# Performance work log

Hardware: AMD Instinct MI355X
Metric: run time of the kernel (lower is better)

The kernel has to match this reference:

```python
import jax, jax.numpy as jnp
import numpy as np

NEG_SLOPE = 0.2

def _gc(inp, adj, W, b):
    # Kipf GraphConvolution: adj @ (inp @ W) + b
    return adj @ (inp @ W) + b

def _lrelu(x):
    return jnp.where(x >= 0, x, NEG_SLOPE * x)

def setup_inputs() -> dict:
    key = jax.random.key(0)
    ks = jax.random.split(key, 24)
    Nx, Ny, Fx, Fy, D1, C = 8192, 4096, 512, 256, 256, 64
    s = 0.05
    inp = {
        "hx1": jax.random.uniform(ks[0], (Nx, Nx), jnp.float32) / Nx,
        "hx2": jax.random.uniform(ks[1], (Nx, Ny), jnp.float32) / Ny,
        "x0": jax.random.normal(ks[2], (Nx, Fx), jnp.float32),
        "hy1": jax.random.uniform(ks[3], (Ny, Ny), jnp.float32) / Ny,
        "hy2": jax.random.uniform(ks[4], (Ny, Nx), jnp.float32) / Nx,
        "y0": jax.random.normal(ks[5], (Ny, Fy), jnp.float32),
        "alpha": jnp.float32(0.6),
        "beta": jnp.float32(0.4),
        # weights/biases of the 8 GraphConvolution layers
        "Wx1a": jax.random.normal(ks[6], (Fx, D1), jnp.float32) * s,
        "bx1a": jnp.zeros((D1,), jnp.float32),
        "Wx1b": jax.random.normal(ks[7], (Fy, D1), jnp.float32) * s,
        "bx1b": jnp.zeros((D1,), jnp.float32),
        "Wx2a": jax.random.normal(ks[8], (D1, C), jnp.float32) * s,
        "bx2a": jnp.zeros((C,), jnp.float32),
        "Wx2b": jax.random.normal(ks[9], (D1, C), jnp.float32) * s,
        "bx2b": jnp.zeros((C,), jnp.float32),
        "Wy1a": jax.random.normal(ks[10], (Fy, D1), jnp.float32) * s,
        "by1a": jnp.zeros((D1,), jnp.float32),
        "Wy1b": jax.random.normal(ks[11], (Fx, D1), jnp.float32) * s,
        "by1b": jnp.zeros((D1,), jnp.float32),
        "Wy2a": jax.random.normal(ks[12], (D1, C), jnp.float32) * s,
        "by2a": jnp.zeros((C,), jnp.float32),
        "Wy2b": jax.random.normal(ks[13], (D1, C), jnp.float32) * s,
        "by2b": jnp.zeros((C,), jnp.float32),
    }
    return inp

def reference(hx1, hx2, x0, hy1, hy2, y0, alpha, beta,
              Wx1a, bx1a, Wx1b, bx1b, Wx2a, bx2a, Wx2b, bx2b,
              Wy1a, by1a, Wy1b, by1b, Wy2a, by2a, Wy2b, by2b):
    # layer 1
    x1 = _lrelu(_gc(x0, hx1, Wx1a, bx1a) * alpha + _gc(y0, hx2, Wx1b, bx1b) * (1 - alpha))
    y1 = _lrelu(_gc(y0, hy1, Wy1a, by1a) * beta + _gc(x0, hy2, Wy1b, by1b) * (1 - beta))
    # layer 2
    x2 = _lrelu(_gc(x1, hx1, Wx2a, bx2a) * alpha + _gc(y1, hx2, Wx2b, bx2b) * (1 - alpha))
    y_pre = _gc(y1, hy1, Wy2a, by2a) * beta + _gc(x1, hy2, Wy2b, by2b) * (1 - beta)
    y2 = _lrelu(y_pre)
    h_hat = jax.nn.sigmoid(x2 @ y2.T)            # [Nx, Ny]
    x_output = jax.nn.log_softmax(x2, axis=1)    # [Nx, nclass]
    return (h_hat, x_output)
```

## Files before the change

kernel.cpp:

```cpp
#include <hip/hip_runtime.h>

typedef unsigned short u16;
typedef unsigned char u8;
typedef long i64;
typedef __attribute__((ext_vector_type(8))) short bf16x8;
typedef __attribute__((ext_vector_type(4))) float f32x4;
typedef __attribute__((ext_vector_type(8))) u16 u16x8;
typedef __attribute__((ext_vector_type(4))) u16 u16x4;
typedef __attribute__((ext_vector_type(4))) float f4;

#define DEVI static __device__ __forceinline__

DEVI u16 f2b(float f) { __bf16 h = (__bf16)f; return __builtin_bit_cast(u16, h); }
DEVI float b2f(u16 h) { unsigned u = ((unsigned)h) << 16; return __builtin_bit_cast(float, u); }

DEVI int pk8(float a, float b, float c, float d) {
  int w = __builtin_amdgcn_cvt_pk_fp8_f32(a, b, 0, false);
  return __builtin_amdgcn_cvt_pk_fp8_f32(c, d, w, true);
}

DEVI void gload16(const void* g, void* l) {
  __builtin_amdgcn_global_load_lds((const __attribute__((address_space(1))) void*)g,
                                   (__attribute__((address_space(3))) void*)l, 16, 0, 0);
}

__global__ __launch_bounds__(1024)
void gemmF_k(const float* __restrict__ xA0, const float* __restrict__ xA1,
             const u8* __restrict__ xB0, const u8* __restrict__ xB1,
             u8* __restrict__ xA0f8, u8* __restrict__ xA1f8,
             int xK0, int xK1, int xL0, int xL1, u16* __restrict__ xC, size_t xMN,
             const float* __restrict__ yA0, const float* __restrict__ yA1,
             const u8* __restrict__ yB0, const u8* __restrict__ yB1,
             u8* __restrict__ yA0f8, u8* __restrict__ yA1f8,
             int yK0, int yK1, int yL0, int yL1, u16* __restrict__ yC, size_t yMN)
{
  constexpr int BM = 128, BK = 64;
  constexpr int LDA = 72;
  constexpr int ASZ = BM * LDA;
  constexpr int BSZ = 256 * BK;
  constexpr int BUFSZ = ASZ + BSZ;
  constexpr float SADJ = 8192.f;
  __shared__ __align__(16) u8 lds[4 * BUFSZ];

  const int tid = threadIdx.x, lane = tid & 63, wave = tid >> 6;
  const int wm = (wave >> 2) * 32, wn = (wave & 3) * 64;
  const int lgrp = lane >> 4, lrow = lane & 15;

  const int flat = blockIdx.x;

  const float *A0, *A1; const u8 *B0, *B1; u8 *A0f8, *A1f8;
  int K0, K1, L0, L1; u16* Cout; size_t MN; int m0, z;
  if (flat < 256) {
    const int s = ((flat & 7) << 5) | (flat >> 3);
    A0=xA0; A1=xA1; B0=xB0; B1=xB1; A0f8=xA0f8; A1f8=xA1f8;
    K0=xK0; K1=xK1; L0=xL0; L1=xL1; Cout=xC; MN=xMN;
    m0 = (s & 63) * BM; z = s >> 6;
  } else {
    const int f2 = flat - 256;
    const int s = ((f2 & 7) << 5) | (f2 >> 3);
    A0=yA0; A1=yA1; B0=yB0; B1=yB1; A0f8=yA0f8; A1f8=yA1f8;
    K0=yK0; K1=yK1; L0=yL0; L1=yL1; Cout=yC; MN=yMN;
    m0 = (s & 31) * BM; z = s >> 5;
  }

  const int nt0 = L0 >> 6, NT = nt0 + (L1 >> 6);

  const int r0 = tid >> 4;
  const int cf = (tid & 15) << 2;

  f32x4 acc[2][4];
#pragma unroll
  for (int m = 0; m < 2; ++m)
#pragma unroll
    for (int n = 0; n < 4; ++n) acc[m][n] = (f32x4){0.f, 0.f, 0.f, 0.f};

  f4 rA0[2], rA1[2];
  int pw0[2], pw1[2];

  auto tileinfo = [&](int t, const float*& Ap, const u8*& Bp, u8*& Af8, int& Kj, int& kk) {
    if (t < nt0) { Ap = A0; Bp = B0; Af8 = A0f8; Kj = K0; kk = z * L0 + (t << 6); }
    else         { Ap = A1; Bp = B1; Af8 = A1f8; Kj = K1; kk = z * L1 + ((t - nt0) << 6); }
  };

  auto loadA = [&](int t, f4 (&r)[2]) {
    const float* Ap; const u8* Bp; u8* Af8; int Kj, kk;
    tileinfo(t, Ap, Bp, Af8, Kj, kk);
#pragma unroll
    for (int j = 0; j < 2; ++j) {
      const int rr = j * 64 + r0;
      r[j] = __builtin_nontemporal_load(
          (const f4*)(Ap + (size_t)(m0 + rr) * Kj + kk + cf));
    }
  };

  auto loadB = [&](int t) {
    const float* Ap; const u8* Bp; u8* Af8; int Kj, kk;
    tileinfo(t, Ap, Bp, Af8, Kj, kk);
    u8* sB = &lds[(t & 3) * BUFSZ] + ASZ;
    const int off = tid * 16;
    const int r = off >> 6, c = off & 63;
    gload16(Bp + (size_t)r * Kj + kk + (c ^ (((r >> 1) & 3) << 4)), sB + off);
  };

  auto writeLDS = [&](int t, f4 (&r)[2], int (&pw)[2]) {
    u8* sA = &lds[(t & 3) * BUFSZ];
#pragma unroll
    for (int j = 0; j < 2; ++j) {
      const int rr = j * 64 + r0;
      pw[j] = pk8(r[j][0] * SADJ, r[j][1] * SADJ, r[j][2] * SADJ, r[j][3] * SADJ);
      *(int*)&sA[rr * LDA + cf] = pw[j];
    }
  };

  auto storeCopy = [&](int t, int (&pw)[2]) {
    const float* Ap; const u8* Bp; u8* Af8; int Kj, kk;
    tileinfo(t, Ap, Bp, Af8, Kj, kk);
#pragma unroll
    for (int j = 0; j < 2; ++j) {
      const int rr = j * 64 + r0;
      *(int*)(Af8 + (size_t)(m0 + rr) * Kj + kk + cf) = pw[j];
    }
  };

  auto compute = [&](int t) {
    const u8* sA = &lds[(t & 3) * BUFSZ];
    const u8* sB = sA + ASZ;
    __builtin_amdgcn_s_setprio(1);
#pragma unroll
    for (int ks = 0; ks < 2; ++ks) {
      i64 a[2], b[4];
#pragma unroll
      for (int m = 0; m < 2; ++m) {
        const int r = wm + m * 16 + lrow;
        a[m] = *(const i64*)&sA[r * LDA + ks * 32 + lgrp * 8];
      }
#pragma unroll
      for (int n = 0; n < 4; ++n) {
        const int r = wn + n * 16 + lrow;
        b[n] = *(const i64*)&sB[r * BK + ((ks * 32 + lgrp * 8) ^ (((r >> 1) & 3) << 4))];
      }
#pragma unroll
      for (int m = 0; m < 2; ++m)
#pragma unroll
        for (int n = 0; n < 4; ++n)
          acc[m][n] = __builtin_amdgcn_mfma_f32_16x16x32_fp8_fp8(a[m], b[n], acc[m][n], 0, 0, 0);
    }
    __builtin_amdgcn_s_setprio(0);
  };

  loadA(0, rA0); loadB(0);
  loadA(1, rA1); loadB(1);

  for (int t = 0; t < NT; t += 2) {
    if (t == 0) asm volatile("s_waitcnt vmcnt(0)" ::: "memory");
    else        asm volatile("s_waitcnt vmcnt(4)" ::: "memory");
    writeLDS(t, rA0, pw0);
    writeLDS(t + 1, rA1, pw1);
    asm volatile("s_waitcnt lgkmcnt(0)" ::: "memory");
    asm volatile("s_barrier" ::: "memory");
    if (t + 2 < NT) { loadA(t + 2, rA0); loadB(t + 2); }
    if (t + 3 < NT) { loadA(t + 3, rA1); loadB(t + 3); }
    storeCopy(t, pw0);
    storeCopy(t + 1, pw1);
    compute(t);
    compute(t + 1);
  }

  u16* Cp = Cout + (size_t)z * MN;
#pragma unroll
  for (int n = 0; n < 4; ++n) {
    const int c = wn + n * 16 + lrow;
#pragma unroll
    for (int m = 0; m < 2; ++m) {
      const int rb = m0 + wm + m * 16 + lgrp * 4;
#pragma unroll
      for (int q = 0; q < 4; ++q)
        Cp[(size_t)(rb + q) * 256 + c] = f2b(acc[m][n][q]);
    }
  }
}

__global__ __launch_bounds__(256)
void gemm8_k(const u8* __restrict__ xA0, const u8* __restrict__ xA1,
             const u8* __restrict__ xB0, const u8* __restrict__ xB1,
             int xK0, int xK1, int xL0, int xL1, u16* __restrict__ xC, size_t xMN,
             const u8* __restrict__ yA0, const u8* __restrict__ yA1,
             const u8* __restrict__ yB0, const u8* __restrict__ yB1,
             int yK0, int yK1, int yL0, int yL1, u16* __restrict__ yC, size_t yMN)
{
  constexpr int BM = 128, BK = 128, BN = 64;
  constexpr int MR = 4, NR = 2;
  constexpr int ASZ = BM * BK, BSZ = BN * BK;
  __shared__ __align__(16) u8 lds[3 * (ASZ + BSZ)];

  const int tid = threadIdx.x, lane = tid & 63, wave = tid >> 6;
  const int wm = (wave >> 1) * 64, wn = (wave & 1) * 32;
  const int lgrp = lane >> 4, lrow = lane & 15;

  const int flat = blockIdx.x;

  const u8 *A0, *A1, *B0, *B1; int K0, K1, L0, L1; u16* Cw; size_t MN;
  int m0, z;
  if (flat < 512) {
    const int s = ((flat & 7) << 6) | (flat >> 3);
    A0=xA0; A1=xA1; B0=xB0; B1=xB1; K0=xK0; K1=xK1; L0=xL0; L1=xL1; Cw=xC; MN=xMN;
    m0 = (s & 63) * BM; z = s >> 6;
  } else {
    const int f2 = flat - 512;
    const int s = ((f2 & 7) << 6) | (f2 >> 3);
    A0=yA0; A1=yA1; B0=yB0; B1=yB1; K0=yK0; K1=yK1; L0=yL0; L1=yL1; Cw=yC; MN=yMN;
    m0 = (s & 31) * BM; z = s >> 5;
  }

  const int nt0 = L0 >> 7, NT = nt0 + (L1 >> 7);

  f32x4 acc[MR][NR];
#pragma unroll
  for (int m = 0; m < MR; ++m)
#pragma unroll
    for (int n = 0; n < NR; ++n) acc[m][n] = (f32x4){0.f, 0.f, 0.f, 0.f};

  auto stage = [&](int buf, int t) {
    const u8* Ap; const u8* Bp; int Kj, kk;
    if (t < nt0) { Ap = A0; Bp = B0; Kj = K0; kk = z * L0 + (t << 7); }
    else         { Ap = A1; Bp = B1; Kj = K1; kk = z * L1 + ((t - nt0) << 7); }
    u8* sA = &lds[buf * (ASZ + BSZ)];
    u8* sB = sA + ASZ;
#pragma unroll
    for (int i = 0; i < ASZ / 4096; ++i) {
      const int off = i * 4096 + tid * 16;
      const int r = off >> 7, c = off & 127;
      gload16(Ap + (size_t)(m0 + r) * Kj + kk + (c ^ ((r & 7) << 4)), sA + off);
    }
#pragma unroll
    for (int i = 0; i < BSZ / 4096; ++i) {
      const int off = i * 4096 + tid * 16;
      const int r = off >> 7, c = off & 127;
      gload16(Bp + (size_t)r * Kj + kk + (c ^ ((r & 7) << 4)), sB + off);
    }
  };

  auto compute = [&](int buf) {
    const u8* sA = &lds[buf * (ASZ + BSZ)];
    const u8* sB = sA + ASZ;
    __builtin_amdgcn_s_setprio(1);
#pragma unroll
    for (int ks = 0; ks < 4; ++ks) {
      i64 a[MR], b[NR];
#pragma unroll
      for (int m = 0; m < MR; ++m) {
        const int r = wm + m * 16 + lrow;
        a[m] = *(const i64*)&sA[r * BK + ((ks * 32 + lgrp * 8) ^ ((r & 7) << 4))];
      }
#pragma unroll
      for (int n = 0; n < NR; ++n) {
        const int r = wn + n * 16 + lrow;
        b[n] = *(const i64*)&sB[r * BK + ((ks * 32 + lgrp * 8) ^ ((r & 7) << 4))];
      }
#pragma unroll
      for (int m = 0; m < MR; ++m)
#pragma unroll
        for (int n = 0; n < NR; ++n)
          acc[m][n] = __builtin_amdgcn_mfma_f32_16x16x32_fp8_fp8(a[m], b[n], acc[m][n], 0, 0, 0);
    }
    __builtin_amdgcn_s_setprio(0);
  };

  stage(0, 0);
  stage(1, 1);
  for (int t = 0; t < NT; ++t) {
    if (t + 1 < NT) asm volatile("s_waitcnt vmcnt(6)" ::: "memory");
    else            asm volatile("s_waitcnt vmcnt(0)" ::: "memory");
    asm volatile("s_barrier" ::: "memory");
    compute(t % 3);
    if (t + 2 < NT) stage((t + 2) % 3, t + 2);
  }

  u16* Cp = Cw + (size_t)z * MN;
#pragma unroll
  for (int n = 0; n < NR; ++n) {
    const int c = wn + n * 16 + lrow;
#pragma unroll
    for (int m = 0; m < MR; ++m) {
      const int rb = m0 + wm + m * 16 + lgrp * 4;
#pragma unroll
      for (int q = 0; q < 4; ++q)
        Cp[(size_t)(rb + q) * 64 + c] = f2b(acc[m][n][q]);
    }
  }
}

template<bool A_F32>
__global__ __launch_bounds__(256)
void gemmS_k(const void* Ax, const u16* Bx, int Kx, int ldcx, u8* Cx1, u8* Cx2,
             const void* Ay, const u16* By, int Ky, int ldcy, u8* Cy1, u8* Cy2,
             int ySplit, int nsplit, float sOut)
{
  constexpr int BM = 64, BN = 64, BK = 32, LD = 40;
  constexpr int MR = 2, NR = 2;
  __shared__ u16 sA[BM * LD];
  __shared__ u16 sB[BN * LD];

  const int tid  = threadIdx.x;
  const int lane = tid & 63;
  const int wave = tid >> 6;
  const int wm = (wave >> 1) * 32;
  const int wn = (wave &  1) * 32;

  const void* A0_; const u16* B0_; int K0, ldc; u8 *C1, *C2; int m0;
  if ((int)blockIdx.y < ySplit) {
    A0_ = Ax; B0_ = Bx; K0 = Kx; ldc = ldcx; C1 = Cx1; C2 = Cx2;
    m0 = blockIdx.y * BM;
  } else {
    A0_ = Ay; B0_ = By; K0 = Ky; ldc = ldcy; C1 = Cy1; C2 = Cy2;
    m0 = (blockIdx.y - ySplit) * BM;
  }
  const int n0 = blockIdx.x * BN;

  constexpr int TPRA = 256 / BM;
  constexpr int EPTA = 32 / TPRA;
  const int ar = tid / TPRA, ac = (tid % TPRA) * EPTA;
  const int br = ar, bc = ac;

  f32x4 acc[MR][NR];
#pragma unroll
  for (int m = 0; m < MR; ++m)
#pragma unroll
    for (int n = 0; n < NR; ++n) acc[m][n] = (f32x4){0.f, 0.f, 0.f, 0.f};

  const int lgrp = lane >> 4, lrow = lane & 15;

  for (int kk = 0; kk < K0; kk += BK) {
    if constexpr (A_F32) {
      const float* Ap = (const float*)A0_ + (size_t)(m0 + ar) * K0 + kk + ac;
      f4 v0 = ((const f4*)Ap)[0];
      f4 v1 = ((const f4*)Ap)[1];
      u16x8 h;
      h[0]=f2b(v0[0]); h[1]=f2b(v0[1]); h[2]=f2b(v0[2]); h[3]=f2b(v0[3]);
      h[4]=f2b(v1[0]); h[5]=f2b(v1[1]); h[6]=f2b(v1[2]); h[7]=f2b(v1[3]);
      *(u16x8*)&sA[ar * LD + ac] = h;
    } else {
      const u16* Ap = (const u16*)A0_ + (size_t)(m0 + ar) * K0 + kk + ac;
      *(u16x8*)&sA[ar * LD + ac] = *(const u16x8*)Ap;
    }
    {
      const u16* Bp = B0_ + (size_t)(n0 + br) * K0 + kk + bc;
      *(u16x8*)&sB[br * LD + bc] = *(const u16x8*)Bp;
    }
    __syncthreads();
    bf16x8 af[MR], bfr[NR];
#pragma unroll
    for (int m = 0; m < MR; ++m)
      af[m] = *(const bf16x8*)&sA[(wm + m * 16 + lrow) * LD + lgrp * 8];
#pragma unroll
    for (int n = 0; n < NR; ++n)
      bfr[n] = *(const bf16x8*)&sB[(wn + n * 16 + lrow) * LD + lgrp * 8];
#pragma unroll
    for (int m = 0; m < MR; ++m)
#pragma unroll
      for (int n = 0; n < NR; ++n)
        acc[m][n] = __builtin_amdgcn_mfma_f32_16x16x32_bf16(af[m], bfr[n], acc[m][n], 0, 0, 0);
    __syncthreads();
  }

#pragma unroll
  for (int n = 0; n < NR; ++n) {
    const int c = n0 + wn + n * 16 + lrow;
    u8* Cp = (c < nsplit) ? C1 : C2;
    const int cr = (c < nsplit) ? c : c - nsplit;
#pragma unroll
    for (int m = 0; m < MR; ++m) {
      const int rb = m0 + wm + m * 16 + lgrp * 4;
      int w = __builtin_amdgcn_cvt_pk_fp8_f32(acc[m][n][0] * sOut, acc[m][n][1] * sOut, 0, false);
      w = __builtin_amdgcn_cvt_pk_fp8_f32(acc[m][n][2] * sOut, acc[m][n][3] * sOut, w, true);
      *(int*)&Cp[(size_t)cr * ldc + rb] = w;
    }
  }
}

__global__ __launch_bounds__(256)
void gemmH_k(const u16* A0_, const u16* B0_, int K0, float* Cout, int ldc)
{
  constexpr int BM = 128, BN = 128, BK = 32, LD = 40;
  constexpr int MR = 4, NR = 4;
  __shared__ u16 sA[BM * LD];
  __shared__ u16 sB[BN * LD];

  const int tid  = threadIdx.x;
  const int lane = tid & 63;
  const int wave = tid >> 6;
  const int wm = (wave >> 1) * 64;
  const int wn = (wave &  1) * 64;
  const int m0 = blockIdx.y * BM;
  const int n0 = blockIdx.x * BN;

  constexpr int TPRA = 2;
  constexpr int EPTA = 16;
  const int ar = tid / TPRA, ac = (tid % TPRA) * EPTA;

  f32x4 acc[MR][NR];
#pragma unroll
  for (int m = 0; m < MR; ++m)
#pragma unroll
    for (int n = 0; n < NR; ++n) acc[m][n] = (f32x4){0.f, 0.f, 0.f, 0.f};

  const int lgrp = lane >> 4, lrow = lane & 15;

  for (int kk = 0; kk < K0; kk += BK) {
    {
      const u16* Ap = A0_ + (size_t)(m0 + ar) * K0 + kk + ac;
      *(u16x8*)&sA[ar * LD + ac]     = ((const u16x8*)Ap)[0];
      *(u16x8*)&sA[ar * LD + ac + 8] = ((const u16x8*)Ap)[1];
      const u16* Bp = B0_ + (size_t)(n0 + ar) * K0 + kk + ac;
      *(u16x8*)&sB[ar * LD + ac]     = ((const u16x8*)Bp)[0];
      *(u16x8*)&sB[ar * LD + ac + 8] = ((const u16x8*)Bp)[1];
    }
    __syncthreads();
    bf16x8 af[MR], bfr[NR];
#pragma unroll
    for (int m = 0; m < MR; ++m)
      af[m] = *(const bf16x8*)&sA[(wm + m * 16 + lrow) * LD + lgrp * 8];
#pragma unroll
    for (int n = 0; n < NR; ++n)
      bfr[n] = *(const bf16x8*)&sB[(wn + n * 16 + lrow) * LD + lgrp * 8];
#pragma unroll
    for (int m = 0; m < MR; ++m)
#pragma unroll
      for (int n = 0; n < NR; ++n)
        acc[m][n] = __builtin_amdgcn_mfma_f32_16x16x32_bf16(af[m], bfr[n], acc[m][n], 0, 0, 0);
    __syncthreads();
  }

  float* Cp = Cout;
#pragma unroll
  for (int n = 0; n < NR; ++n) {
    const int c = n0 + wn + n * 16 + lrow;
#pragma unroll
    for (int m = 0; m < MR; ++m) {
      const int rb = m0 + wm + m * 16 + lgrp * 4;
#pragma unroll
      for (int q = 0; q < 4; ++q)
        __builtin_nontemporal_store(1.f / (1.f + __expf(-acc[m][n][q])),
                                    &Cp[(size_t)(rb + q) * ldc + c]);
    }
  }
}

__global__ __launch_bounds__(256)
void combine1_k(const u16* __restrict__ partX, const u16* __restrict__ partY,
                int xBlocks, size_t MNx, size_t MNy, int KSx_, int KSy_,
                const float* bxa, const float* bxb, const float* ap,
                const float* bya, const float* byb, const float* bp,
                u16* x1, u16* y1, float invs)
{
  const u16* parts; size_t MN; int KS, nb, bid = blockIdx.x;
  const float *b0, *b1, *mixp; u16* out;
  if (bid < xBlocks) {
    parts = partX; MN = MNx; KS = KSx_; b0 = bxa; b1 = bxb; mixp = ap; out = x1; nb = xBlocks;
  } else {
    bid -= xBlocks;
    parts = partY; MN = MNy; KS = KSy_; b0 = bya; b1 = byb; mixp = bp; out = y1;
    nb = gridDim.x - xBlocks;
  }
  const float mix = *mixp;
  const size_t stride = (size_t)nb * 1024;
  for (size_t i = ((size_t)bid * 256 + threadIdx.x) * 4; i < MN; i += stride) {
    f4 s = {0.f, 0.f, 0.f, 0.f};
    for (int zz = 0; zz < KS; ++zz) {
      u16x4 pv = *(const u16x4*)&parts[(size_t)zz * MN + i];
#pragma unroll
      for (int q = 0; q < 4; ++q) s[q] += b2f(pv[q]);
    }
    const int c = (int)(i & 255);
    u16x4 o;
#pragma unroll
    for (int q = 0; q < 4; ++q) {
      float v = s[q] * invs + mix * b0[c + q] + (1.f - mix) * b1[c + q];
      v = v >= 0.f ? v : 0.2f * v;
      o[q] = f2b(v);
    }
    *(u16x4*)&out[i] = o;
  }
}

__global__ __launch_bounds__(256)
void combine2_k(const u16* __restrict__ partX, const u16* __restrict__ partY,
                int xRowBlocks, size_t MNx, size_t MNy,
                const float* bxa, const float* bxb, const float* ap,
                const float* bya, const float* byb, const float* bp,
                u16* x2, u16* y2, float* xout, float invs)
{
  const int w = threadIdx.x >> 6, lane = threadIdx.x & 63;
  if ((int)blockIdx.x < xRowBlocks) {
    const int row = blockIdx.x * 4 + w;
    const float a = *ap;
    float s = 0.f;
#pragma unroll
    for (int z = 0; z < 8; ++z)
      s += b2f(partX[(size_t)z * MNx + (size_t)row * 64 + lane]);
    float v = s * invs + a * bxa[lane] + (1.f - a) * bxb[lane];
    v = v >= 0.f ? v : 0.2f * v;
    x2[(size_t)row * 64 + lane] = f2b(v);
    float m = v;
#pragma unroll
    for (int o = 32; o; o >>= 1) m = fmaxf(m, __shfl_xor(m, o));
    float t = __expf(v - m);
#pragma unroll
    for (int o = 32; o; o >>= 1) t += __shfl_xor(t, o);
    xout[(size_t)row * 64 + lane] = v - m - __logf(t);
  } else {
    const int row = ((int)blockIdx.x - xRowBlocks) * 4 + w;
    const float b = *bp;
    float s = 0.f;
#pragma unroll
    for (int z = 0; z < 16; ++z)
      s += b2f(partY[(size_t)z * MNy + (size_t)row * 64 + lane]);
    float v = s * invs + b * bya[lane] + (1.f - b) * byb[lane];
    v = v >= 0.f ? v : 0.2f * v;
    y2[(size_t)row * 64 + lane] = f2b(v);
  }
}

__global__ __launch_bounds__(256)
void prep_w(const float* Wx1a, const float* Wx1b, const float* Wy1a, const float* Wy1b,
            const float* Wx2a, const float* Wx2b, const float* Wy2a, const float* Wy2b,
            u16* WtX, u16* WtY, u16* W2X, u16* W2Y,
            const float* ap, const float* bp)
{
  const int zz = blockIdx.z;
  const float a = *ap, b = *bp;
  const float* W; u16* O; int K, N, roff; float s;
  switch (zz) {
    case 0: W=Wx1a; O=WtX; K=512; N=256; roff=0;   s=a;      break;
    case 1: W=Wy1b; O=WtX; K=512; N=256; roff=256; s=1.f-b;  break;
    case 2: W=Wx1b; O=WtY; K=256; N=256; roff=0;   s=1.f-a;  break;
    case 3: W=Wy1a; O=WtY; K=256; N=256; roff=256; s=b;      break;
    case 4: W=Wx2a; O=W2X; K=256; N=64;  roff=0;   s=a;      break;
    case 5: W=Wy2b; O=W2X; K=256; N=64;  roff=64;  s=1.f-b;  break;
    case 6: W=Wx2b; O=W2Y; K=256; N=64;  roff=0;   s=1.f-a;  break;
    default:W=Wy2a; O=W2Y; K=256; N=64;  roff=64;  s=b;      break;
  }
  const int total = K * N;
  for (int i = blockIdx.x * 256 + threadIdx.x; i < total; i += gridDim.x * 256) {
    const int k = i / N, n = i - k * N;
    O[(size_t)(n + roff) * K + k] = f2b(W[i] * s);
  }
}

extern "C" void kernel_launch(void* const* d_in, const int* in_sizes, int n_in,
                              void* d_out, int out_size, void* d_ws, size_t ws_size,
                              hipStream_t stream)
{
  const float* hx1 = (const float*)d_in[0];
  const float* hx2 = (const float*)d_in[1];
  const float* x0  = (const float*)d_in[2];
  const float* hy1 = (const float*)d_in[3];
  const float* hy2 = (const float*)d_in[4];
  const float* y0  = (const float*)d_in[5];
  const float* alphap = (const float*)d_in[6];
  const float* betap  = (const float*)d_in[7];
  const float* Wx1a = (const float*)d_in[8];  const float* bx1a = (const float*)d_in[9];
  const float* Wx1b = (const float*)d_in[10]; const float* bx1b = (const float*)d_in[11];
  const float* Wx2a = (const float*)d_in[12]; const float* bx2a = (const float*)d_in[13];
  const float* Wx2b = (const float*)d_in[14]; const float* bx2b = (const float*)d_in[15];
  const float* Wy1a = (const float*)d_in[16]; const float* by1a = (const float*)d_in[17];
  const float* Wy1b = (const float*)d_in[18]; const float* by1b = (const float*)d_in[19];
  const float* Wy2a = (const float*)d_in[20]; const float* by2a = (const float*)d_in[21];
  const float* Wy2b = (const float*)d_in[22]; const float* by2b = (const float*)d_in[23];
  (void)in_sizes; (void)n_in; (void)out_size;

  constexpr int Nx = 8192, Ny = 4096, Fx = 512, Fy = 256, D1 = 256, C = 64;
  constexpr float SB1 = 16.f, SB2 = 256.f;
  constexpr float INV1 = 1.f / (8192.f * 16.f);
  constexpr float INV2 = 1.f / (8192.f * 256.f);
  constexpr int KSx = 4, KSy = 8;

  u8* wsb = (u8*)d_ws;
  size_t off = 0;
  auto alloc = [&](size_t n) { u8* p = wsb + off; off += (n + 63) & ~(size_t)63; return p; };

  u16* WtX = (u16*)alloc((size_t)512 * 512 * 2);
  u16* WtY = (u16*)alloc((size_t)512 * 256 * 2);
  u16* W2X = (u16*)alloc((size_t)128 * 256 * 2);
  u16* W2Y = (u16*)alloc((size_t)128 * 256 * 2);
  u8* B1x  = alloc((size_t)D1 * Nx);
  u8* B2x  = alloc((size_t)D1 * Ny);
  u8* B1y  = alloc((size_t)D1 * Ny);
  u8* B2y  = alloc((size_t)D1 * Nx);
  u16* x1  = (u16*)alloc((size_t)Nx * D1 * 2);
  u16* y1  = (u16*)alloc((size_t)Ny * D1 * 2);
  u8* B1x2 = alloc((size_t)C * Nx);
  u8* B2x2 = alloc((size_t)C * Ny);
  u8* B1y2 = alloc((size_t)C * Ny);
  u8* B2y2 = alloc((size_t)C * Nx);
  u16* x2  = (u16*)alloc((size_t)Nx * C * 2);
  u16* y2  = (u16*)alloc((size_t)Ny * C * 2);

  const size_t base_off = off;
  const size_t szHx1 = (size_t)Nx * Nx, szHx2 = (size_t)Nx * Ny;
  const size_t szHy1 = (size_t)Ny * Ny, szHy2 = (size_t)Ny * Nx;
  const size_t needA = base_off + szHx1 + szHx2 + szHy1 + szHy2 + ((size_t)32 << 20) + (1 << 20);

  u8 *hx1f8, *hx2f8, *hy1f8, *hy2f8; u16* part;
  if (ws_size >= needA) {
    hx1f8 = alloc(szHx1); hx2f8 = alloc(szHx2);
    hy1f8 = alloc(szHy1); hy2f8 = alloc(szHy2);
    part  = (u16*)alloc((size_t)32 << 20);
  } else {
    hy1f8 = alloc(szHy1); hy2f8 = alloc(szHy2);
    hx1f8 = (u8*)d_out;
    hx2f8 = (u8*)d_out + szHx1;
    part  = (u16*)((u8*)d_out + szHx1 + szHx2);
  }

  const size_t MNx1 = (size_t)Nx * D1, MNy1 = (size_t)Ny * D1;
  const size_t MNx2 = (size_t)Nx * C,  MNy2 = (size_t)Ny * C;
  u16* partY1 = part + (size_t)KSx * MNx1;
  u16* partY2 = part + 8 * MNx2;

  prep_w<<<dim3(256, 1, 8), 256, 0, stream>>>(Wx1a, Wx1b, Wy1a, Wy1b, Wx2a, Wx2b, Wy2a, Wy2b,
      WtX, WtY, W2X, W2Y, alphap, betap);

  gemmS_k<true><<<dim3(8, Nx/64 + Ny/64), 256, 0, stream>>>(
      x0, WtX, Fx, Nx, B1x, B2y,
      y0, WtY, Fy, Ny, B2x, B1y,
      Nx/64, 256, SB1);

  gemmF_k<<<dim3(512), 1024, 0, stream>>>(
      hx1, hx2, B1x, B2x, hx1f8, hx2f8, Nx, Ny, Nx/KSx, Ny/KSx, part, MNx1,
      hy1, hy2, B1y, B2y, hy1f8, hy2f8, Ny, Nx, Ny/KSy, Nx/KSy, partY1, MNy1);

  combine1_k<<<dim3(3072), 256, 0, stream>>>(part, partY1, 2048, MNx1, MNy1, KSx, KSy,
      bx1a, bx1b, alphap, by1a, by1b, betap, x1, y1, INV1);

  gemmS_k<false><<<dim3(2, Nx/64 + Ny/64), 256, 0, stream>>>(
      x1, W2X, D1, Nx, B1x2, B2y2,
      y1, W2Y, D1, Ny, B2x2, B1y2,
      Nx/64, 64, SB2);

  gemm8_k<<<dim3(1024), 256, 0, stream>>>(
      hx1f8, hx2f8, B1x2, B2x2, Nx, Ny, 1024, 512, part, MNx2,
      hy1f8, hy2f8, B1y2, B2y2, Ny, Nx, 256, 512, partY2, MNy2);

  combine2_k<<<dim3(2048 + 1024), 256, 0, stream>>>(part, partY2, 2048, MNx2, MNy2,
      bx2a, bx2b, alphap, by2a, by2b, betap, x2, y2,
      (float*)d_out + (size_t)Nx * Ny, INV2);

  gemmH_k<<<dim3(Ny/128, Nx/128), 256, 0, stream>>>(x2, y2, C, (float*)d_out, Ny);
}
```

Baseline: 305.3 us.

## Deepen gemmF prefetch to three-stage superstep pipeline with six LDS buffers

Restructures the fused fp32-to-fp8 adjacency GEMM main loop into supersteps of two K-tiles. Each superstep prefetches the A and B data for the superstep two ahead, using three rotating register banks and six LDS buffers instead of four. The vmcnt waits are retuned to match the number of loads and stores in flight. The goal is to hide more global-memory latency on the streaming adjacency reads. In exchange it uses more registers and nearly all of the LDS, and it assumes the number of supersteps is a multiple of three.

```diff
diff --git a/kernel.cpp b/kernel.cpp
--- a/kernel.cpp
+++ b/kernel.cpp
@@ -40,7 +40,7 @@
   constexpr int BSZ = 256 * BK;
   constexpr int BUFSZ = ASZ + BSZ;
   constexpr float SADJ = 8192.f;
-  __shared__ __align__(16) u8 lds[4 * BUFSZ];
+  __shared__ __align__(16) u8 lds[6 * BUFSZ];
 
   const int tid = threadIdx.x, lane = tid & 63, wave = tid >> 6;
   const int wm = (wave >> 2) * 32, wn = (wave & 3) * 64;
@@ -64,6 +64,7 @@
   }
 
   const int nt0 = L0 >> 6, NT = nt0 + (L1 >> 6);
+  const int NSS = NT >> 1;
 
   const int r0 = tid >> 4;
   const int cf = (tid & 15) << 2;
@@ -74,7 +75,7 @@
 #pragma unroll
     for (int n = 0; n < 4; ++n) acc[m][n] = (f32x4){0.f, 0.f, 0.f, 0.f};
 
-  f4 rA0[2], rA1[2];
+  f4 bk0[4], bk1[4], bk2[4];
   int pw0[2], pw1[2];
 
   auto tileinfo = [&](int t, const float*& Ap, const u8*& Bp, u8*& Af8, int& Kj, int& kk) {
@@ -82,28 +83,34 @@
     else         { Ap = A1; Bp = B1; Af8 = A1f8; Kj = K1; kk = z * L1 + ((t - nt0) << 6); }
   };
 
-  auto loadA = [&](int t, f4 (&r)[2]) {
-    const float* Ap; const u8* Bp; u8* Af8; int Kj, kk;
-    tileinfo(t, Ap, Bp, Af8, Kj, kk);
-#pragma unroll
-    for (int j = 0; j < 2; ++j) {
-      const int rr = j * 64 + r0;
-      r[j] = __builtin_nontemporal_load(
-          (const f4*)(Ap + (size_t)(m0 + rr) * Kj + kk + cf));
-    }
-  };
-
   auto loadB = [&](int t) {
     const float* Ap; const u8* Bp; u8* Af8; int Kj, kk;
     tileinfo(t, Ap, Bp, Af8, Kj, kk);
-    u8* sB = &lds[(t & 3) * BUFSZ] + ASZ;
+    u8* sB = &lds[(t % 6) * BUFSZ] + ASZ;
     const int off = tid * 16;
     const int r = off >> 6, c = off & 63;
     gload16(Bp + (size_t)r * Kj + kk + (c ^ (((r >> 1) & 3) << 4)), sB + off);
   };
 
-  auto writeLDS = [&](int t, f4 (&r)[2], int (&pw)[2]) {
-    u8* sA = &lds[(t & 3) * BUFSZ];
+  auto loadPair = [&](int p, f4 (&bk)[4]) {
+    const int t0 = 2 * p;
+#pragma unroll
+    for (int h = 0; h < 2; ++h) {
+      const int t = t0 + h;
+      const float* Ap; const u8* Bp; u8* Af8; int Kj, kk;
+      tileinfo(t, Ap, Bp, Af8, Kj, kk);
+#pragma unroll
+      for (int j = 0; j < 2; ++j) {
+        const int rr = j * 64 + r0;
+        bk[h * 2 + j] = __builtin_nontemporal_load(
+            (const f4*)(Ap + (size_t)(m0 + rr) * Kj + kk + cf));
+      }
+      loadB(t);
+    }
+  };
+
+  auto writeLDS = [&](int t, f4* r, int (&pw)[2]) {
+    u8* sA = &lds[(t % 6) * BUFSZ];
 #pragma unroll
     for (int j = 0; j < 2; ++j) {
       const int rr = j * 64 + r0;
@@ -123,7 +130,7 @@
   };
 
   auto compute = [&](int t) {
-    const u8* sA = &lds[(t & 3) * BUFSZ];
+    const u8* sA = &lds[(t % 6) * BUFSZ];
     const u8* sB = sA + ASZ;
     __builtin_amdgcn_s_setprio(1);
 #pragma unroll
@@ -148,22 +155,30 @@
     __builtin_amdgcn_s_setprio(0);
   };
 
-  loadA(0, rA0); loadB(0);
-  loadA(1, rA1); loadB(1);
-
-  for (int t = 0; t < NT; t += 2) {
-    if (t == 0) asm volatile("s_waitcnt vmcnt(0)" ::: "memory");
-    else        asm volatile("s_waitcnt vmcnt(4)" ::: "memory");
-    writeLDS(t, rA0, pw0);
-    writeLDS(t + 1, rA1, pw1);
+  auto superstep = [&](int p, f4 (&cur)[4], f4 (&nxt)[4]) {
+    const int t = 2 * p;
+    if (p == NSS - 1)      asm volatile("s_waitcnt vmcnt(0)"  ::: "memory");
+    else if (p == 0)       asm volatile("s_waitcnt vmcnt(6)"  ::: "memory");
+    else if (p == 1)       asm volatile("s_waitcnt vmcnt(10)" ::: "memory");
+    else                   asm volatile("s_waitcnt vmcnt(14)" ::: "memory");
+    writeLDS(t,     &cur[0], pw0);
+    writeLDS(t + 1, &cur[2], pw1);
     asm volatile("s_waitcnt lgkmcnt(0)" ::: "memory");
     asm volatile("s_barrier" ::: "memory");
-    if (t + 2 < NT) { loadA(t + 2, rA0); loadB(t + 2); }
-    if (t + 3 < NT) { loadA(t + 3, rA1); loadB(t + 3); }
+    if (p + 2 < NSS) loadPair(p + 2, nxt);
     storeCopy(t, pw0);
     storeCopy(t + 1, pw1);
     compute(t);
     compute(t + 1);
+  };
+
+  loadPair(0, bk0);
+  loadPair(1, bk1);
+
+  for (int p = 0; p < NSS; p += 3) {
+    superstep(p,     bk0, bk2);
+    superstep(p + 1, bk1, bk0);
+    superstep(p + 2, bk2, bk1);
   }
 
   u16* Cp = Cout + (size_t)z * MN;
```

Result: slower. 374.7 us (+22.7%).
